# Optimization experiments

Hardware: AMD Instinct MI355X
Metric: run time of the kernel (lower is better)

## Reference

```python
import jax, jax.numpy as jnp
import numpy as np

NUM_BLKS = 6
H = 4
D = 64

def _ln(x, g, b, eps=1e-6):
    m = jnp.mean(x, -1, keepdims=True)
    v = jnp.mean((x - m) ** 2, -1, keepdims=True)
    return (x - m) * jax.lax.rsqrt(v + eps) * g + b

def _mlp3(x, W1, b1, W2, b2, W3, b3):
    h = jax.nn.gelu(x @ W1 + b1)
    h = jax.nn.gelu(h @ W2 + b2)
    return h @ W3 + b3

def _attn(q, kv, bias, kmask, Wq, Wk, Wv, Wo):
    B, Nq, Dm = q.shape
    Dh = Dm // H
    Q = (q @ Wq).reshape(B, Nq, H, Dh)
    K = (kv @ Wk).reshape(B, -1, H, Dh)
    V = (kv @ Wv).reshape(B, -1, H, Dh)
    logits = jnp.einsum('bqhd,bkhd->bhqk', Q, K) / jnp.sqrt(jnp.float32(Dh))
    logits = logits + bias[:, None]  # additive similarity-kernel bias
    logits = jnp.where(kmask[:, None, None, :], logits, -1e9)
    a = jax.nn.softmax(logits, -1)
    o = jnp.einsum('bhqk,bkhd->bqhd', a, V).reshape(B, Nq, Dm)
    return o @ Wo

def _bias(sim, p):
    # learned RBF-style bias; non-finite similarities masked to 0 (mirrors isfinite mask)
    return jnp.where(jnp.isfinite(sim), p[0] * jnp.exp(-sim * jax.nn.softplus(p[1])), 0.0)

def _forward(s_ctx, t_ctx, f_ctx, s_test, t_test, emb_obs, ea_W1, ea_b1, ea_W2, ea_b2, ea_W3, ea_b3, norm_g, norm_b, blk_Wq, blk_Wk, blk_Wv, blk_Wo, blk_ln1_g, blk_ln1_b, blk_ff_W1, blk_ff_b1, blk_ff_W2, blk_ff_b2, blk_ln2_g, blk_ln2_b, sbias_p, tbias_p, fnorm_g, fnorm_b, head_W1, head_b1, head_W2, head_b2, head_W3, head_b3, mask_ctx):
    B, NC, _ = f_ctx.shape
    NT = s_test.shape[1]
    obs_e = jnp.broadcast_to(emb_obs[1], (B, NC, emb_obs.shape[-1]))    # obs=1 embedding
    unobs_e = jnp.broadcast_to(emb_obs[0], (B, NT, emb_obs.shape[-1]))  # unobs=0 embedding
    f_test = jnp.zeros((B, NT, f_ctx.shape[-1]), f_ctx.dtype)
    ctx = jnp.concatenate([obs_e, s_ctx, t_ctx, f_ctx], -1)    # [B,NC,8]
    test = jnp.concatenate([unobs_e, s_test, t_test, f_test], -1)  # [B,NT,8]
    kvs = _ln(_mlp3(ctx, ea_W1, ea_b1, ea_W2, ea_b2, ea_W3, ea_b3), norm_g, norm_b)
    qvs = _ln(_mlp3(test, ea_W1, ea_b1, ea_W2, ea_b2, ea_W3, ea_b3), norm_g, norm_b)
    # pairwise similarity kernels (vmap over batch expressed via broadcasting)
    s_qk = jnp.sum((s_test[:, :, None] - s_ctx[:, None]) ** 2, -1)  # [B,NT,NC]
    s_kk = jnp.sum((s_ctx[:, :, None] - s_ctx[:, None]) ** 2, -1)   # [B,NC,NC]
    t_qk = jnp.abs(t_test[..., 0][:, :, None] - t_ctx[..., 0][:, None, :])
    t_kk = jnp.abs(t_ctx[..., 0][:, :, None] - t_ctx[..., 0][:, None, :])

    def _block(x, kv, bias, i):
        a = _attn(x, kv, bias, mask_ctx, blk_Wq[i], blk_Wk[i], blk_Wv[i], blk_Wo[i])
        x = _ln(x + a, blk_ln1_g[i], blk_ln1_b[i])
        h = jax.nn.gelu(x @ blk_ff_W1[i] + blk_ff_b1[i]) @ blk_ff_W2[i] + blk_ff_b2[i]
        return _ln(x + h, blk_ln2_g[i], blk_ln2_b[i])

    for i in range(NUM_BLKS):
        qk_b = _bias(s_qk, sbias_p[i]) + _bias(t_qk, tbias_p[i])
        kk_b = _bias(s_kk, sbias_p[i]) + _bias(t_kk, tbias_p[i])
        kvs = _block(kvs, kvs, kk_b, i)   # context self-attention
        qvs = _block(qvs, kvs, qk_b, i)   # test -> context cross-attention
    qvs = _ln(qvs, fnorm_g, fnorm_b)
    out = _mlp3(qvs, head_W1, head_b1, head_W2, head_b2, head_W3, head_b3)  # [B,NT,2]
    mean = out[..., :1]
    std = jax.nn.softplus(out[..., 1:]) + 1e-3  # DiagonalMVN params
    return jnp.concatenate([mean, std], -1)

def setup_inputs() -> dict:
    key = jax.random.key(0)
    ks = iter(jax.random.split(key, 48))
    rn = lambda *s: jax.random.normal(next(ks), s, jnp.float32)
    B, NC, NT = 8, 1024, 1024
    return dict(
        s_ctx=rn(B, NC, 2), t_ctx=rn(B, NC, 1), f_ctx=rn(B, NC, 1),
        mask_ctx=jnp.ones((B, NC), bool),
        s_test=rn(B, NT, 2), t_test=rn(B, NT, 1),
        emb_obs=rn(2, 4) * 0.02,
        ea_W1=rn(8, 256) * 0.05, ea_b1=jnp.zeros(256),
        ea_W2=rn(256, 128) * 0.05, ea_b2=jnp.zeros(128),
        ea_W3=rn(128, 64) * 0.05, ea_b3=jnp.zeros(64),
        norm_g=jnp.ones(64), norm_b=jnp.zeros(64),
        blk_Wq=rn(NUM_BLKS, D, D) * 0.05, blk_Wk=rn(NUM_BLKS, D, D) * 0.05,
        blk_Wv=rn(NUM_BLKS, D, D) * 0.05, blk_Wo=rn(NUM_BLKS, D, D) * 0.05,
        blk_ln1_g=jnp.ones((NUM_BLKS, D)), blk_ln1_b=jnp.zeros((NUM_BLKS, D)),
        blk_ff_W1=rn(NUM_BLKS, D, 4 * D) * 0.05, blk_ff_b1=jnp.zeros((NUM_BLKS, 4 * D)),
        blk_ff_W2=rn(NUM_BLKS, 4 * D, D) * 0.05, blk_ff_b2=jnp.zeros((NUM_BLKS, D)),
        blk_ln2_g=jnp.ones((NUM_BLKS, D)), blk_ln2_b=jnp.zeros((NUM_BLKS, D)),
        sbias_p=rn(NUM_BLKS, 2) * 0.5, tbias_p=rn(NUM_BLKS, 2) * 0.5,
        fnorm_g=jnp.ones(64), fnorm_b=jnp.zeros(64),
        head_W1=rn(64, 256) * 0.05, head_b1=jnp.zeros(256),
        head_W2=rn(256, 64) * 0.05, head_b2=jnp.zeros(64),
        head_W3=rn(64, 2) * 0.05, head_b3=jnp.zeros(2),
    )

def reference(s_ctx, t_ctx, f_ctx, mask_ctx, s_test, t_test, emb_obs, ea_W1, ea_b1, ea_W2, ea_b2, ea_W3, ea_b3, norm_g, norm_b, blk_Wq, blk_Wk, blk_Wv, blk_Wo, blk_ln1_g, blk_ln1_b, blk_ff_W1, blk_ff_b1, blk_ff_W2, blk_ff_b2, blk_ln2_g, blk_ln2_b, sbias_p, tbias_p, fnorm_g, fnorm_b, head_W1, head_b1, head_W2, head_b2, head_W3, head_b3):
    return _forward(s_ctx, t_ctx, f_ctx, s_test, t_test, emb_obs, ea_W1, ea_b1, ea_W2, ea_b2, ea_W3, ea_b3, norm_g, norm_b, blk_Wq, blk_Wk, blk_Wv, blk_Wo, blk_ln1_g, blk_ln1_b, blk_ff_W1, blk_ff_b1, blk_ff_W2, blk_ff_b2, blk_ln2_g, blk_ln2_b, sbias_p, tbias_p, fnorm_g, fnorm_b, head_W1, head_b1, head_W2, head_b2, head_W3, head_b3, mask_ctx)
```

## Files before the change

### kernel.cpp

```cpp
#include <hip/hip_runtime.h>
#include <hip/hip_bf16.h>

typedef __hip_bfloat16 bf16;

#define BB 8
#define NN 1024
#define HH 4

typedef __attribute__((ext_vector_type(4))) short s4v;
typedef __attribute__((ext_vector_type(4))) float f4v;
typedef __attribute__((ext_vector_type(8))) unsigned short us8v;

__device__ inline float b2f(bf16 x){ return __bfloat162float(x); }
__device__ inline float us2f(unsigned short u){
  union { unsigned int i; float f; } c; c.i = ((unsigned int)u) << 16; return c.f;
}
__device__ inline unsigned short f2us(float x){
  __hip_bfloat16 h = __float2bfloat16(x);
  union { __hip_bfloat16 h; unsigned short u; } c; c.h = h; return c.u;
}
__device__ inline float wsum(float v){
#pragma unroll
  for(int m=32;m>0;m>>=1) v += __shfl_xor(v,m,64);
  return v;
}
__device__ inline float tanh_f(float u){
  float e = __expf(-2.f*fabsf(u));
  float r = (1.f-e)/(1.f+e);
  return u < 0.f ? -r : r;
}
__device__ inline float gelu_f(float x){
  float u = 0.7978845608028654f*(x + 0.044715f*x*x*x);
  return 0.5f*x*(1.f+tanh_f(u));
}
__device__ inline float softplus_f(float x){
  return fmaxf(x,0.f) + log1pf(__expf(-fabsf(x)));
}

__global__ __launch_bounds__(256) void k_detect(const unsigned short* __restrict__ w,
                                                int n, int* __restrict__ flag){
  __shared__ int s;
  if(threadIdx.x==0) s=0;
  __syncthreads();
  int bad=0;
  for(int i=threadIdx.x;i<n;i+=256){
    float x = us2f(w[i]);
    if(!(fabsf(x) < 1000.f)) bad=1;
  }
  if(bad) atomicOr(&s,1);
  __syncthreads();
  if(threadIdx.x==0) *flag = s;
}

#define NSEG 36
struct ConvArgs {
  const void* src[NSEG];
  int dstoff[NSEG];
  int cum[NSEG+1];
};

__global__ __launch_bounds__(256) void k_convert(ConvArgs a, const int* __restrict__ flag,
                                                 unsigned short* __restrict__ dst){
  int f = *flag;
  int T = a.cum[NSEG];
  for(int i = blockIdx.x*256 + threadIdx.x; i < T; i += gridDim.x*256){
    int lo=0, hi=NSEG-1;
    while(lo<hi){ int mid=(lo+hi)>>1; if(i >= a.cum[mid+1]) lo=mid+1; else hi=mid; }
    int j = i - a.cum[lo];
    unsigned short v;
    if(f) v = f2us(((const float*)a.src[lo])[j]);
    else  v = ((const unsigned short*)a.src[lo])[j];
    dst[a.dstoff[lo] + j] = v;
  }
}

__global__ __launch_bounds__(256) void k_embed3(
    const bf16* __restrict__ s_ctx, const bf16* __restrict__ t_ctx, const bf16* __restrict__ f_ctx,
    const bf16* __restrict__ s_test, const bf16* __restrict__ t_test, const bf16* __restrict__ emb,
    const bf16* __restrict__ W1, const bf16* __restrict__ b1,
    const bf16* __restrict__ W2, const bf16* __restrict__ b2,
    const bf16* __restrict__ W3, const bf16* __restrict__ b3,
    const bf16* __restrict__ g, const bf16* __restrict__ bb,
    float* __restrict__ kvs, float* __restrict__ qvs)
{
  __shared__ float xs[32*8];
  __shared__ unsigned short h1b[32*264];
  __shared__ unsigned short h2b[32*136];
  __shared__ unsigned short wch[64*132];
  __shared__ unsigned short w3s[128*68];
  int tid=threadIdx.x, wv=tid>>6, lane=tid&63;
  int c=lane&15, quad=lane>>4;
  int tok0 = blockIdx.x*32;
  const f4v z4 = {0.f,0.f,0.f,0.f};

  {
    int t=tid>>3, i=tid&7;
    int tok=tok0+t;
    bool cx = tok < BB*NN; int n = cx? tok : tok-BB*NN;
    float v;
    if(i<4) v = b2f(emb[(cx?4:0)+i]);
    else if(i==4) v = b2f(cx? s_ctx[n*2] : s_test[n*2]);
    else if(i==5) v = b2f(cx? s_ctx[n*2+1] : s_test[n*2+1]);
    else if(i==6) v = b2f(cx? t_ctx[n] : t_test[n]);
    else v = cx? b2f(f_ctx[n]) : 0.f;
    xs[t*8+i]=v;
  }
  {
    const unsigned short* w3u=(const unsigned short*)W3;
    for(int v=tid; v<2048; v+=256){
      int k=v>>4, n4=(v&15)*4;
      ushort4 w = *(const ushort4*)&w3u[k*64+n4];
      *(ushort4*)&w3s[k*68+n4] = w;
    }
  }
  __syncthreads();

  {
    float w1r[8][4], b1r[4];
#pragma unroll
    for(int j=0;j<4;j++) b1r[j]=b2f(b1[lane+64*j]);
#pragma unroll
    for(int i=0;i<8;i++)
#pragma unroll
      for(int j=0;j<4;j++) w1r[i][j]=b2f(W1[i*256+lane+64*j]);
    for(int t=0;t<8;t++){
// ... 88 lines not shown
      float d=y-m;
      float vv=wsum(d*d)*(1.f/64.f);
      float o=d*rsqrtf(vv+1e-6f)*gg+b0;
      bool cx = tok<BB*NN; int bn = cx? tok : tok-BB*NN;
      (cx?kvs:qvs)[bn*64+lane]=o;
    }
  }
}

__global__ __launch_bounds__(256) void k_proj4(
  const float* __restrict__ x, const float* __restrict__ q2,
  const bf16* __restrict__ Wq, const bf16* __restrict__ Wk, const bf16* __restrict__ Wv,
  unsigned short* __restrict__ qA, unsigned short* __restrict__ kA,
  unsigned short* __restrict__ vA, unsigned short* __restrict__ qB)
{
  __shared__ float wq[4096], wk[4096], wv[4096];
  __shared__ float xs[1024], qs[1024];
  int tid = threadIdx.x;
  for(int v=tid; v<1536; v+=256){
    int m = v>>9;
    int idx = (v & 511) * 8;
    const unsigned short* src = (m==0)?(const unsigned short*)Wq
                              :((m==1)?(const unsigned short*)Wk:(const unsigned short*)Wv);
    us8v w = *(const us8v*)&src[idx];
    float* dst = (m==0)?wq:((m==1)?wk:wv);
#pragma unroll
    for(int e=0;e<8;e++) dst[idx+e] = us2f((unsigned short)w[e]);
  }
  int base = blockIdx.x*16;
  ((float4*)xs)[tid] = ((const float4*)(x  + (size_t)base*64))[tid];
  ((float4*)qs)[tid] = ((const float4*)(q2 + (size_t)base*64))[tid];
  __syncthreads();
  int wave=tid>>6, lane=tid&63;
  int h=lane>>4, dh=lane&15;
#pragma unroll
  for(int t=0;t<4;t++){
    int tl = wave*4+t;
    int tok = base+tl;
    int b = tok>>10, n = tok&1023;
    float aq=0.f, ak=0.f, av=0.f, aq2=0.f;
    for(int k=0;k<64;k++){
      float xv = xs[tl*64+k], qv = qs[tl*64+k];
      float wqv = wq[k*64+lane];
      aq += xv*wqv;
      ak += xv*wk[k*64+lane];
      av += xv*wv[k*64+lane];
      aq2 += qv*wqv;
    }
    int o = ((b*HH + h)*NN + n)*16 + dh;
    qA[o]=f2us(aq); kA[o]=f2us(ak); vA[o]=f2us(av); qB[o]=f2us(aq2);
  }
}

#define TSP 72
#define HSP 264
__global__ __launch_bounds__(256) void k_layer(
  const float* __restrict__ x,
  const unsigned short* __restrict__ qbh, const unsigned short* __restrict__ kbh,
  const unsigned short* __restrict__ vbh,
  const bf16* __restrict__ sq, const bf16* __restrict__ tq,
  const bf16* __restrict__ sk, const bf16* __restrict__ tk,
  const bf16* __restrict__ sp, const bf16* __restrict__ tp,
  const bf16* __restrict__ Wo, const bf16* __restrict__ g1, const bf16* __restrict__ b1,
  const bf16* __restrict__ W1, const bf16* __restrict__ fb1,
  const bf16* __restrict__ W2, const bf16* __restrict__ fb2,
  const bf16* __restrict__ g2, const bf16* __restrict__ b2g,
  float* __restrict__ xout, int mode,
  const bf16* __restrict__ Wm0, const bf16* __restrict__ Wm1,
  const bf16* __restrict__ Wm2, const bf16* __restrict__ Wm3,
  const bf16* __restrict__ Wm4,
  unsigned short* __restrict__ O0, unsigned short* __restrict__ O1,
  unsigned short* __restrict__ O2, unsigned short* __restrict__ O3,
  unsigned short* __restrict__ O4)
{
  __shared__ f4v arena4[3072];
  __shared__ unsigned short wos[4096];
  __shared__ float un[1024];
  __shared__ float ts[1024];
  __shared__ unsigned short tsb[16*TSP];
  __shared__ unsigned short hsb[16*HSP];
  __shared__ float ls[64];
  __shared__ float lmrg[4][16][4];
  unsigned short* arena_us = (unsigned short*)arena4;
  float* omrg = (float*)arena4;
  unsigned short* wbuf = arena_us + 8192;
  unsigned short* skbx = arena_us + 20480;
  unsigned short* skby = skbx + 1024;
  unsigned short* skbt = skby + 1024;

  int tid=threadIdx.x, wave=tid>>6, lane=tid&63;
  int c=lane&15, quad=lane>>4;
  int base = blockIdx.x*16;
  int b = base>>10, n0 = base&1023;
  const f4v z4 = {0.f,0.f,0.f,0.f};

  {
    const unsigned short* wou=(const unsigned short*)Wo;
    ((us8v*)wos)[tid] = ((const us8v*)wou)[tid];
    ((us8v*)wos)[tid+256] = ((const us8v*)wou)[tid+256];
    const unsigned short* usk=(const unsigned short*)sk;
    const unsigned short* utk=(const unsigned short*)tk;
    for(int i2=tid;i2<1024;i2+=256){
      int kg = b*NN + i2;
      skbx[i2]=usk[kg*2]; skby[i2]=usk[kg*2+1]; skbt[i2]=utk[kg];
    }
  }

  int qi = b*NN + n0 + c;
  float p0s=b2f(sp[0]), p1s=softplus_f(b2f(sp[1]));
  float p0t=b2f(tp[0]), p1t=softplus_f(b2f(tp[1]));
  float sq0=b2f(sq[qi*2]), sq1=b2f(sq[qi*2+1]), tq0=b2f(tq[qi]);
  s4v qf[4];
#pragma unroll
  for(int h=0;h<4;h++)
    qf[h] = *(const s4v*)(qbh + (size_t)((b*HH+h)*NN + n0 + c)*16 + quad*4);

  unsigned short* kstW = arena_us + wave*5120;
  unsigned short* vstW = kstW + 2560;

  f4v oacc[4]={z4,z4,z4,z4};
  float lacc[4]={0.f,0.f,0.f,0.f};

  ushort4 krg[2][4], vrg[2][4];
#pragma unroll
  for(int j=0;j<2;j++){
    int idx=lane+64*j; int h=idx>>5, key=idx&31;
    size_t src = ((size_t)(b*HH+h)*NN + wave*256 + key)*16;
    const ushort4* kp=(const ushort4*)(kbh+src);
    const ushort4* vp=(const ushort4*)(vbh+src);
#pragma unroll
    for(int e=0;e<4;e++){ krg[j][e]=kp[e]; vrg[j][e]=vp[e]; }
  }
  __syncthreads();

  for(int st=0; st<8; ++st){
    asm volatile("s_waitcnt lgkmcnt(0)" ::: "memory");
#pragma unroll
    for(int j=0;j<2;j++){
      int idx=lane+64*j; int h=idx>>5, key=idx&31;
      ushort4* kd = (ushort4*)&kstW[h*640 + key*20];
      kd[0]=krg[j][0]; kd[1]=krg[j][1]; kd[2]=krg[j][2]; kd[3]=krg[j][3];
      unsigned short* vd = &vstW[h*640 + key];
      vd[ 0*40]=vrg[j][0].x; vd[ 1*40]=vrg[j][0].y; vd[ 2*40]=vrg[j][0].z; vd[ 3*40]=vrg[j][0].w;
      vd[ 4*40]=vrg[j][1].x; vd[ 5*40]=vrg[j][1].y; vd[ 6*40]=vrg[j][1].z; vd[ 7*40]=vrg[j][1].w;
      vd[ 8*40]=vrg[j][2].x; vd[ 9*40]=vrg[j][2].y; vd[10*40]=vrg[j][2].z; vd[11*40]=vrg[j][2].w;
      vd[12*40]=vrg[j][3].x; vd[13*40]=vrg[j][3].y; vd[14*40]=vrg[j][3].z; vd[15*40]=vrg[j][3].w;
    }
    if(st<7){
#pragma unroll
      for(int j=0;j<2;j++){
        int idx=lane+64*j; int h=idx>>5, key=idx&31;
        size_t src = ((size_t)(b*HH+h)*NN + wave*256 + (st+1)*32 + key)*16;
        const ushort4* kp=(const ushort4*)(kbh+src);
        const ushort4* vp=(const ushort4*)(vbh+src);
#pragma unroll
        for(int e=0;e<4;e++){ krg[j][e]=kp[e]; vrg[j][e]=vp[e]; }
      }
    }
    asm volatile("s_waitcnt lgkmcnt(0)" ::: "memory");
    __builtin_amdgcn_sched_barrier(0);
#pragma unroll
    for(int t2=0;t2<2;t2++){
      int kk = st*32 + t2*16;
      float bias[4];
#pragma unroll
      for(int r=0;r<4;r++){
        int kix = wave*256 + kk + quad*4 + r;
        float d0 = sq0-us2f(skbx[kix]), d1 = sq1-us2f(skby[kix]);
        float dt = fabsf(tq0-us2f(skbt[kix]));
        bias[r] = p0s*__expf(-(d0*d0+d1*d1)*p1s) + p0t*__expf(-dt*p1t);
      }
#pragma unroll
      for(int h=0;h<4;h++){
        s4v kf = *(const s4v*)&kstW[h*640 + (t2*16+c)*20 + quad*4];
        f4v s = __builtin_amdgcn_mfma_f32_16x16x16bf16_1k(kf, qf[h], z4, 0,0,0);
        float p0 = __expf(fminf(s[0]*0.25f + bias[0], 60.f));
        float p1 = __expf(fminf(s[1]*0.25f + bias[1], 60.f));
        float p2 = __expf(fminf(s[2]*0.25f + bias[2], 60.f));
        float p3 = __expf(fminf(s[3]*0.25f + bias[3], 60.f));
        lacc[h] += (p0+p1)+(p2+p3);
        s4v pf;
        pf.x=(short)f2us(p0); pf.y=(short)f2us(p1);
        pf.z=(short)f2us(p2); pf.w=(short)f2us(p3);
        s4v vf = *(const s4v*)&vstW[h*640 + c*40 + t2*16 + quad*4];
        oacc[h] = __builtin_amdgcn_mfma_f32_16x16x16bf16_1k(vf, pf, oacc[h], 0,0,0);
      }
    }
  }

  __syncthreads();
#pragma unroll
  for(int h=0;h<4;h++){
    lacc[h] += __shfl_xor(lacc[h],16,64);
    lacc[h] += __shfl_xor(lacc[h],32,64);
  }
#pragma unroll
  for(int h=0;h<4;h++)
    *(f4v*)&omrg[(wave*16+c)*64 + h*16 + quad*4] = oacc[h];
  if(quad==0){
#pragma unroll
    for(int h=0;h<4;h++) lmrg[wave][c][h]=lacc[h];
  }
  {
    const unsigned short* w1u=(const unsigned short*)W1;
#pragma unroll
    for(int j=0;j<8;j++)
      ((us8v*)wbuf)[tid + j*256] = ((const us8v*)w1u)[tid + j*256];
  }
  __syncthreads();
  if(tid<64){
    int tl=tid>>2, h=tid&3;
    ls[tid] = lmrg[0][tl][h]+lmrg[1][tl][h]+lmrg[2][tl][h]+lmrg[3][tl][h];
  }
  __syncthreads();
#pragma unroll
  for(int j=0;j<4;j++){
    int i = j*256+tid;
    int tl=i>>6, hd=i&63;
    float o = omrg[tl*64+hd] + omrg[(16+tl)*64+hd]
            + omrg[(32+tl)*64+hd] + omrg[(48+tl)*64+hd];
    un[i] = o / ls[(tl<<2)|(hd>>4)];
  }
  __syncthreads();

  {
    float xr[4];
#pragma unroll
    for(int t=0;t<4;t++) xr[t] = x[(size_t)(base+wave*4+t)*64 + lane];
    float acc[4]={0.f,0.f,0.f,0.f};
    for(int k=0;k<64;k++){
      float w = us2f(wos[k*64+lane]);
      acc[0] += un[(wave*4+0)*64+k]*w;
      acc[1] += un[(wave*4+1)*64+k]*w;
      acc[2] += un[(wave*4+2)*64+k]*w;
      acc[3] += un[(wave*4+3)*64+k]*w;
    }
    float gg=b2f(g1[lane]), bbv=b2f(b1[lane]);
#pragma unroll
    for(int t=0;t<4;t++){
      float y = xr[t] + acc[t];
      float mm = wsum(y)*(1.f/64.f);
      float d = y-mm;
      float v = wsum(d*d)*(1.f/64.f);
      float tt = d*rsqrtf(v+1e-6f)*gg + bbv;
      ts[(wave*4+t)*64+lane] = tt;
      tsb[(wave*4+t)*TSP+lane] = f2us(tt);
    }
  }
  __syncthreads();

  {
    s4v af[4];
#pragma unroll
    for(int ks=0;ks<4;ks++)
      af[ks] = *(const s4v*)&tsb[c*TSP + ks*16 + quad*4];
#pragma unroll
    for(int tile=0;tile<4;tile++){
      int n0t = wave*64 + tile*16;
      f4v acc = z4;
#pragma unroll
      for(int ks=0;ks<4;ks++){
        int kb = ks*16 + quad*4;
        s4v bfv;
        bfv.x = (short)wbuf[(kb+0)*256 + n0t + c];
        bfv.y = (short)wbuf[(kb+1)*256 + n0t + c];
        bfv.z = (short)wbuf[(kb+2)*256 + n0t + c];
        bfv.w = (short)wbuf[(kb+3)*256 + n0t + c];
        acc = __builtin_amdgcn_mfma_f32_16x16x16bf16_1k(af[ks], bfv, acc, 0,0,0);
      }
      float bias = b2f(fb1[n0t + c]);
#pragma unroll
      for(int r=0;r<4;r++){
        int tok = quad*4 + r;
        hsb[tok*HSP + n0t + c] = f2us(gelu_f(acc[r] + bias));
      }
    }
  }
  __syncthreads();
  {
    const unsigned short* w2u=(const unsigned short*)W2;
#pragma unroll
    for(int j=0;j<8;j++)
      ((us8v*)wbuf)[tid + j*256] = ((const us8v*)w2u)[tid + j*256];
  }
  __syncthreads();

  {
    int n0t = wave*16;
    f4v acc = z4;
#pragma unroll
    for(int ks=0;ks<16;ks++){
      s4v af = *(const s4v*)&hsb[c*HSP + ks*16 + quad*4];
      int kb = ks*16 + quad*4;
      s4v bfv;
      bfv.x = (short)wbuf[(kb+0)*64 + n0t + c];
      bfv.y = (short)wbuf[(kb+1)*64 + n0t + c];
      bfv.z = (short)wbuf[(kb+2)*64 + n0t + c];
      bfv.w = (short)wbuf[(kb+3)*64 + n0t + c];
      acc = __builtin_amdgcn_mfma_f32_16x16x16bf16_1k(af, bfv, acc, 0,0,0);
    }
    float bias = b2f(fb2[n0t + c]);
#pragma unroll
    for(int r=0;r<4;r++)
      un[(quad*4+r)*64 + n0t + c] = acc[r] + bias;
  }
  __syncthreads();

  {
    float gg=b2f(g2[lane]), b0=b2f(b2g[lane]);
#pragma unroll
    for(int t=0;t<4;t++){
      float y = ts[(wave*4+t)*64+lane] + un[(wave*4+t)*64+lane];
      float mm = wsum(y)*(1.f/64.f);
      float d = y-mm;
      float v = wsum(d*d)*(1.f/64.f);
      float yo = d*rsqrtf(v+1e-6f)*gg + b0;
      xout[(size_t)(base+wave*4+t)*64+lane] = yo;
      ts[(wave*4+t)*64+lane] = yo;
    }
  }
  __syncthreads();

  if(mode==0){
#pragma unroll
    for(int j=0;j<2;j++){
      ((us8v*)wbuf)[tid + j*256       ] = ((const us8v*)(const unsigned short*)Wm0)[tid + j*256];
      ((us8v*)wbuf)[tid + j*256 +  512] = ((const us8v*)(const unsigned short*)Wm1)[tid + j*256];
      ((us8v*)wbuf)[tid + j*256 + 1024] = ((const us8v*)(const unsigned short*)Wm2)[tid + j*256];
      ((us8v*)wbuf)[tid + j*256 + 1536] = ((const us8v*)(const unsigned short*)Wm3)[tid + j*256];
      ((us8v*)wos )[tid + j*256       ] = ((const us8v*)(const unsigned short*)Wm4)[tid + j*256];
    }
  } else {
#pragma unroll
    for(int j=0;j<2;j++)
      ((us8v*)wos)[tid + j*256] = ((const us8v*)(const unsigned short*)Wm0)[tid + j*256];
  }
  __syncthreads();

  {
    int h=lane>>4, dh=lane&15;
    if(mode==0){
      float a0[4],a1[4],a2[4],a3[4],a4[4];
#pragma unroll
      for(int t=0;t<4;t++){ a0[t]=0.f;a1[t]=0.f;a2[t]=0.f;a3[t]=0.f;a4[t]=0.f; }
      for(int k=0;k<64;k++){
        float w0=us2f(wbuf[k*64+lane]);
        float w1=us2f(wbuf[4096+k*64+lane]);
        float w2=us2f(wbuf[8192+k*64+lane]);
        float w3=us2f(wbuf[12288+k*64+lane]);
        float w4=us2f(wos[k*64+lane]);
#pragma unroll
        for(int t=0;t<4;t++){
          float tv = ts[(wave*4+t)*64+k];
          a0[t]+=tv*w0; a1[t]+=tv*w1; a2[t]+=tv*w2; a3[t]+=tv*w3; a4[t]+=tv*w4;
        }
      }
#pragma unroll
      for(int t=0;t<4;t++){
        int tok = base+wave*4+t;
        int bq=tok>>10, n=tok&1023;
        int o = ((bq*HH+h)*NN+n)*16+dh;
        O0[o]=f2us(a0[t]); O1[o]=f2us(a1[t]); O2[o]=f2us(a2[t]);
        O3[o]=f2us(a3[t]); O4[o]=f2us(a4[t]);
      }
    } else {
      float a0[4]={0.f,0.f,0.f,0.f};
      for(int k=0;k<64;k++){
        float w0=us2f(wos[k*64+lane]);
#pragma unroll
        for(int t=0;t<4;t++) a0[t] += ts[(wave*4+t)*64+k]*w0;
      }
#pragma unroll
      for(int t=0;t<4;t++){
        int tok = base+wave*4+t;
        int bq=tok>>10, n=tok&1023;
        int o = ((bq*HH+h)*NN+n)*16+dh;
        O0[o]=f2us(a0[t]);
      }
    }
  }
}

__global__ __launch_bounds__(256) void k_head2(
  const float* __restrict__ qvs,
  const bf16* __restrict__ fng, const bf16* __restrict__ fnb,
  const bf16* __restrict__ W1, const bf16* __restrict__ b1,
  const bf16* __restrict__ W2, const bf16* __restrict__ b2,
  const bf16* __restrict__ W3, const bf16* __restrict__ b3,
  void* __restrict__ out, const int* __restrict__ flag)
{
  __shared__ unsigned short wbuf[16384];
  __shared__ float xls[1024];
  __shared__ float hh1[4096];
  int tid=threadIdx.x, wave=tid>>6, lane=tid&63;
  int base = blockIdx.x*16;
  {
    const unsigned short* w1u=(const unsigned short*)W1;
#pragma unroll
    for(int j=0;j<8;j++)
      ((us8v*)wbuf)[tid + j*256] = ((const us8v*)w1u)[tid + j*256];
  }
  {
    float gg=b2f(fng[lane]), bb=b2f(fnb[lane]);
#pragma unroll
    for(int t=0;t<4;t++){
      int tl=wave*4+t;
      float xv = qvs[(size_t)(base+tl)*64+lane];
      float m = wsum(xv)*(1.f/64.f);
      float d = xv-m;
      float v = wsum(d*d)*(1.f/64.f);
      xls[tl*64+lane] = d*rsqrtf(v+1e-6f)*gg + bb;
    }
  }
  __syncthreads();
  {
    float a0[4],a1[4],a2[4],a3[4];
    float bb0=b2f(b1[lane*4+0]), bb1v=b2f(b1[lane*4+1]),
          bb2v=b2f(b1[lane*4+2]), bb3=b2f(b1[lane*4+3]);
#pragma unroll
    for(int t=0;t<4;t++){ a0[t]=bb0; a1[t]=bb1v; a2[t]=bb2v; a3[t]=bb3; }
    for(int k=0;k<64;k++){
      ushort4 w = *(const ushort4*)&wbuf[k*256+lane*4];
      float w0=us2f(w.x), w1=us2f(w.y), w2=us2f(w.z), w3=us2f(w.w);
#pragma unroll
      for(int t=0;t<4;t++){
        float tv = xls[(wave*4+t)*64+k];
        a0[t]+=tv*w0; a1[t]+=tv*w1; a2[t]+=tv*w2; a3[t]+=tv*w3;
      }
    }
#pragma unroll
// ... 51 lines not shown

  ConvArgs ca;
  int cur = 0;
  int off[NSEG];
  {
    int cum = 0;
    for(int k=0;k<NSEG;k++){
      int n = in_sizes[idxs[k]];
      ca.src[k] = d_in[idxs[k]];
      ca.dstoff[k] = cur;
      ca.cum[k] = cum;
      off[k] = cur;
      cur += (n + 15) & ~15;
      cum += n;
    }
    ca.cum[NSEG] = cum;
  }
  size_t convEnd = 64 + (size_t)cur*2;
  size_t fbaseOff = (convEnd + 255) & ~255ULL;
  float* fbase = (float*)((char*)d_ws + fbaseOff);

  const bf16* P[NSEG];
  for(int k=0;k<NSEG;k++) P[k] = (const bf16*)(conv + off[k]);
  const bf16* s_ctx =P[0];  const bf16* t_ctx =P[1];  const bf16* f_ctx =P[2];
  const bf16* s_test=P[3];  const bf16* t_test=P[4];  const bf16* emb   =P[5];
  const bf16* eaW1=P[6];   const bf16* eab1=P[7];
  const bf16* eaW2=P[8];   const bf16* eab2=P[9];
  const bf16* eaW3=P[10];  const bf16* eab3=P[11];
  const bf16* ng=P[12];    const bf16* nb=P[13];
  const bf16* bWq=P[14];   const bf16* bWk=P[15];
  const bf16* bWv=P[16];   const bf16* bWo=P[17];
  const bf16* l1g=P[18];   const bf16* l1b=P[19];
  const bf16* fW1=P[20];   const bf16* fb1=P[21];
  const bf16* fW2=P[22];   const bf16* fb2=P[23];
  const bf16* l2g=P[24];   const bf16* l2b=P[25];
  const bf16* sbp=P[26];   const bf16* tbp=P[27];
  const bf16* fng=P[28];   const bf16* fnb=P[29];
  const bf16* hW1=P[30];   const bf16* hb1=P[31];
  const bf16* hW2=P[32];   const bf16* hb2=P[33];
  const bf16* hW3=P[34];   const bf16* hb3=P[35];

  float* kvs = fbase;
  float* qvs = fbase + 524288;
  unsigned short* qA0 = (unsigned short*)(fbase + 1048576);
  unsigned short* kA0 = (unsigned short*)(fbase + 1310720);
  unsigned short* vA0 = (unsigned short*)(fbase + 1572864);
  unsigned short* qB0 = (unsigned short*)(fbase + 1835008);
  unsigned short* kB  = (unsigned short*)(fbase + 2097152);
  unsigned short* vB  = (unsigned short*)(fbase + 2359296);
  unsigned short* qA1 = (unsigned short*)(fbase + 2621440);
  unsigned short* kA1 = (unsigned short*)(fbase + 2883584);
  unsigned short* vA1 = (unsigned short*)(fbase + 3145728);
  unsigned short* qB1 = (unsigned short*)(fbase + 3407872);

  k_detect<<<1,256,0,stream>>>((const unsigned short*)d_in[7], in_sizes[7], flagp);
  k_convert<<<512,256,0,stream>>>(ca, flagp, conv);
  k_embed3<<<512,256,0,stream>>>(s_ctx,t_ctx,f_ctx,s_test,t_test,emb,
                                 eaW1,eab1,eaW2,eab2,eaW3,eab3,ng,nb,kvs,qvs);
  k_proj4<<<512,256,0,stream>>>(kvs,qvs,bWq,bWk,bWv,qA0,kA0,vA0,qB0);

  unsigned short *qAc=qA0,*kAc=kA0,*vAc=vA0,*qBc=qB0;
  unsigned short *qAn=qA1,*kAn=kA1,*vAn=vA1,*qBn=qB1;

  for(int i=0;i<6;i++){
    int nx = (i<5)? i+1 : 5;
    const bf16* Wo=bWo+i*4096;
    const bf16* g1=l1g+i*64;   const bf16* b1=l1b+i*64;
    const bf16* W1=fW1+i*16384; const bf16* bb1=fb1+i*256;
    const bf16* W2=fW2+i*16384; const bf16* bb2=fb2+i*64;
    const bf16* g2=l2g+i*64;   const bf16* b2=l2b+i*64;
    const bf16* spi=sbp+i*2;   const bf16* tpi=tbp+i*2;
    const bf16* Wk_i=bWk+i*4096; const bf16* Wv_i=bWv+i*4096;
    const bf16* Wq_n=bWq+nx*4096; const bf16* Wk_n=bWk+nx*4096; const bf16* Wv_n=bWv+nx*4096;

    k_layer<<<512,256,0,stream>>>(kvs, qAc,kAc,vAc,
                                  s_ctx,t_ctx,s_ctx,t_ctx,spi,tpi,
                                  Wo,g1,b1,W1,bb1,W2,bb2,g2,b2, kvs, 0,
                                  Wk_i,Wv_i,Wq_n,Wk_n,Wv_n,
                                  kB,vB,qAn,kAn,vAn);
    k_layer<<<512,256,0,stream>>>(qvs, qBc,kB,vB,
                                  s_test,t_test,s_ctx,t_ctx,spi,tpi,
                                  Wo,g1,b1,W1,bb1,W2,bb2,g2,b2, qvs, 1,
                                  Wq_n,Wq_n,Wq_n,Wq_n,Wq_n,
                                  qBn,qBn,qBn,qBn,qBn);
    unsigned short* t;
    t=qAc; qAc=qAn; qAn=t;
    t=kAc; kAc=kAn; kAn=t;
    t=vAc; vAc=vAn; vAn=t;
    t=qBc; qBc=qBn; qBn=t;
  }
  k_head2<<<512,256,0,stream>>>(qvs,fng,fnb,hW1,hb1,hW2,hb2,hW3,hb3,d_out,flagp);
}
```

Measured before the change: 603.5 us.

## Pre-transpose swizzled layer weights, use MFMA for projections, and double block size to 512

```diff
diff --git a/kernel.cpp b/kernel.cpp
--- a/kernel.cpp
+++ b/kernel.cpp
@@ -71,6 +71,40 @@
     if(f) v = f2us(((const float*)a.src[lo])[j]);
     else  v = ((const unsigned short*)a.src[lo])[j];
     dst[a.dstoff[lo] + j] = v;
+  }
+}
+
+__global__ __launch_bounds__(256) void k_prep(
+  const bf16* __restrict__ Wo6, const bf16* __restrict__ Wq6,
+  const bf16* __restrict__ Wk6, const bf16* __restrict__ Wv6,
+  const bf16* __restrict__ W16, const bf16* __restrict__ W26,
+  unsigned short* __restrict__ out)
+{
+  int l = blockIdx.x / 6, m = blockIdx.x % 6;
+  int tid = threadIdx.x;
+  unsigned short* dst = out + l*49152;
+  if(m < 4){
+    const unsigned short* src = (const unsigned short*)
+      (m==0? Wo6 + l*4096 : m==1? Wq6 + l*4096 : m==2? Wk6 + l*4096 : Wv6 + l*4096);
+    unsigned short* d = dst + m*4096;
+    for(int e=tid; e<4096; e+=256){
+      int n = e>>6, k = e&63;
+      d[n*64 + (k ^ ((n&15)<<2))] = src[k*64 + n];
+    }
+  } else if(m==4){
+    const unsigned short* src = (const unsigned short*)(W16 + l*16384);
+    unsigned short* d = dst + 16384;
+    for(int e=tid; e<16384; e+=256){
+      int n = e>>6, k = e&63;
+      d[n*64 + (k ^ ((n&15)<<2))] = src[k*256 + n];
+    }
+  } else {
+    const unsigned short* src = (const unsigned short*)(W26 + l*16384);
+    unsigned short* d = dst + 32768;
+    for(int e=tid; e<16384; e+=256){
+      int n = e>>8, k = e&255;
+      d[n*256 + (k ^ ((n&15)<<2))] = src[k*64 + n];
+    }
   }
 }
 
@@ -265,37 +299,39 @@
   }
 }
 
-#define TSP 72
-#define HSP 264
-__global__ __launch_bounds__(256) void k_layer(
+#define HSP 260
+__global__ __launch_bounds__(512, 4) void k_layer(
   const float* __restrict__ x,
   const unsigned short* __restrict__ qbh, const unsigned short* __restrict__ kbh,
   const unsigned short* __restrict__ vbh,
   const bf16* __restrict__ sq, const bf16* __restrict__ tq,
   const bf16* __restrict__ sk, const bf16* __restrict__ tk,
   const bf16* __restrict__ sp, const bf16* __restrict__ tp,
-  const bf16* __restrict__ Wo, const bf16* __restrict__ g1, const bf16* __restrict__ b1,
-  const bf16* __restrict__ W1, const bf16* __restrict__ fb1,
-  const bf16* __restrict__ W2, const bf16* __restrict__ fb2,
+  const unsigned short* __restrict__ WoT,
+  const bf16* __restrict__ g1, const bf16* __restrict__ b1,
+  const unsigned short* __restrict__ W1T, const bf16* __restrict__ fb1,
+  const unsigned short* __restrict__ W2T, const bf16* __restrict__ fb2,
   const bf16* __restrict__ g2, const bf16* __restrict__ b2g,
   float* __restrict__ xout, int mode,
-  const bf16* __restrict__ Wm0, const bf16* __restrict__ Wm1,
-  const bf16* __restrict__ Wm2, const bf16* __restrict__ Wm3,
-  const bf16* __restrict__ Wm4,
+  const unsigned short* __restrict__ Wm0, const unsigned short* __restrict__ Wm1,
+  const unsigned short* __restrict__ Wm2, const unsigned short* __restrict__ Wm3,
+  const unsigned short* __restrict__ Wm4,
   unsigned short* __restrict__ O0, unsigned short* __restrict__ O1,
   unsigned short* __restrict__ O2, unsigned short* __restrict__ O3,
   unsigned short* __restrict__ O4)
 {
   __shared__ f4v arena4[3072];
   __shared__ unsigned short wos[4096];
-  __shared__ float un[1024];
   __shared__ float ts[1024];
-  __shared__ unsigned short tsb[16*TSP];
-  __shared__ unsigned short hsb[16*HSP];
+  __shared__ float lmrg[8][16][4];
   __shared__ float ls[64];
-  __shared__ float lmrg[4][16][4];
   unsigned short* arena_us = (unsigned short*)arena4;
   float* omrg = (float*)arena4;
+  unsigned short* unb = (unsigned short*)ts;
+  float* unWf = (float*)(arena_us + 3136);
+  unsigned short* hsb = arena_us;
+  float* unFf = (float*)(arena_us + 4160);
+  unsigned short* tsb = arena_us + 6240;
   unsigned short* wbuf = arena_us + 8192;
   unsigned short* skbx = arena_us + 20480;
   unsigned short* skby = skbx + 1024;
@@ -303,89 +339,77 @@
 
   int tid=threadIdx.x, wave=tid>>6, lane=tid&63;
   int c=lane&15, quad=lane>>4;
-  int base = blockIdx.x*16;
-  int b = base>>10, n0 = base&1023;
+  int base=blockIdx.x*16, bq=base>>10, ntok=base&1023;
   const f4v z4 = {0.f,0.f,0.f,0.f};
 
   {
-    const unsigned short* wou=(const unsigned short*)Wo;
-    ((us8v*)wos)[tid] = ((const us8v*)wou)[tid];
-    ((us8v*)wos)[tid+256] = ((const us8v*)wou)[tid+256];
+    ((us8v*)wos)[tid] = ((const us8v*)WoT)[tid];
     const unsigned short* usk=(const unsigned short*)sk;
     const unsigned short* utk=(const unsigned short*)tk;
-    for(int i2=tid;i2<1024;i2+=256){
-      int kg = b*NN + i2;
+    for(int i2=tid;i2<1024;i2+=512){
+      int kg = bq*NN + i2;
       skbx[i2]=usk[kg*2]; skby[i2]=usk[kg*2+1]; skbt[i2]=utk[kg];
     }
   }
 
-  int qi = b*NN + n0 + c;
+  int qi = bq*NN + ntok + c;
   float p0s=b2f(sp[0]), p1s=softplus_f(b2f(sp[1]));
   float p0t=b2f(tp[0]), p1t=softplus_f(b2f(tp[1]));
   float sq0=b2f(sq[qi*2]), sq1=b2f(sq[qi*2+1]), tq0=b2f(tq[qi]);
   s4v qf[4];
 #pragma unroll
   for(int h=0;h<4;h++)
-    qf[h] = *(const s4v*)(qbh + (size_t)((b*HH+h)*NN + n0 + c)*16 + quad*4);
-
-  unsigned short* kstW = arena_us + wave*5120;
-  unsigned short* vstW = kstW + 2560;
+    qf[h] = *(const s4v*)(qbh + (size_t)((bq*HH+h)*NN + ntok + c)*16 + quad*4);
+
+  unsigned short* kstW = arena_us + wave*2560;
+  unsigned short* vstW = kstW + 1280;
 
   f4v oacc[4]={z4,z4,z4,z4};
   float lacc[4]={0.f,0.f,0.f,0.f};
 
-  ushort4 krg[2][4], vrg[2][4];
-#pragma unroll
-  for(int j=0;j<2;j++){
-    int idx=lane+64*j; int h=idx>>5, key=idx&31;
-    size_t src = ((size_t)(b*HH+h)*NN + wave*256 + key)*16;
+  int hs = lane>>4, ky = lane&15;
+  ushort4 krg[4], vrg[4];
+  {
+    size_t src = ((size_t)(bq*HH+hs)*NN + wave*128 + ky)*16;
     const ushort4* kp=(const ushort4*)(kbh+src);
     const ushort4* vp=(const ushort4*)(vbh+src);
 #pragma unroll
-    for(int e=0;e<4;e++){ krg[j][e]=kp[e]; vrg[j][e]=vp[e]; }
+    for(int e=0;e<4;e++){ krg[e]=kp[e]; vrg[e]=vp[e]; }
   }
   __syncthreads();
 
   for(int st=0; st<8; ++st){
     asm volatile("s_waitcnt lgkmcnt(0)" ::: "memory");
-#pragma unroll
-    for(int j=0;j<2;j++){
-      int idx=lane+64*j; int h=idx>>5, key=idx&31;
-      ushort4* kd = (ushort4*)&kstW[h*640 + key*20];
-      kd[0]=krg[j][0]; kd[1]=krg[j][1]; kd[2]=krg[j][2]; kd[3]=krg[j][3];
-      unsigned short* vd = &vstW[h*640 + key];
-      vd[ 0*40]=vrg[j][0].x; vd[ 1*40]=vrg[j][0].y; vd[ 2*40]=vrg[j][0].z; vd[ 3*40]=vrg[j][0].w;
-      vd[ 4*40]=vrg[j][1].x; vd[ 5*40]=vrg[j][1].y; vd[ 6*40]=vrg[j][1].z; vd[ 7*40]=vrg[j][1].w;
-      vd[ 8*40]=vrg[j][2].x; vd[ 9*40]=vrg[j][2].y; vd[10*40]=vrg[j][2].z; vd[11*40]=vrg[j][2].w;
-      vd[12*40]=vrg[j][3].x; vd[13*40]=vrg[j][3].y; vd[14*40]=vrg[j][3].z; vd[15*40]=vrg[j][3].w;
+    {
+      ushort4* kd = (ushort4*)&kstW[hs*320 + ky*20];
+      kd[0]=krg[0]; kd[1]=krg[1]; kd[2]=krg[2]; kd[3]=krg[3];
+      unsigned short* vd = &vstW[hs*320 + ky];
+      vd[ 0*20]=vrg[0].x; vd[ 1*20]=vrg[0].y; vd[ 2*20]=vrg[0].z; vd[ 3*20]=vrg[0].w;
+      vd[ 4*20]=vrg[1].x; vd[ 5*20]=vrg[1].y; vd[ 6*20]=vrg[1].z; vd[ 7*20]=vrg[1].w;
+      vd[ 8*20]=vrg[2].x; vd[ 9*20]=vrg[2].y; vd[10*20]=vrg[2].z; vd[11*20]=vrg[2].w;
+      vd[12*20]=vrg[3].x; vd[13*20]=vrg[3].y; vd[14*20]=vrg[3].z; vd[15*20]=vrg[3].w;
     }
     if(st<7){
-#pragma unroll
-      for(int j=0;j<2;j++){
-        int idx=lane+64*j; int h=idx>>5, key=idx&31;
-        size_t src = ((size_t)(b*HH+h)*NN + wave*256 + (st+1)*32 + key)*16;
-        const ushort4* kp=(const ushort4*)(kbh+src);
-        const ushort4* vp=(const ushort4*)(vbh+src);
-#pragma unroll
-        for(int e=0;e<4;e++){ krg[j][e]=kp[e]; vrg[j][e]=vp[e]; }
-      }
+      size_t src = ((size_t)(bq*HH+hs)*NN + wave*128 + (st+1)*16 + ky)*16;
+      const ushort4* kp=(const ushort4*)(kbh+src);
+      const ushort4* vp=(const ushort4*)(vbh+src);
+#pragma unroll
+      for(int e=0;e<4;e++){ krg[e]=kp[e]; vrg[e]=vp[e]; }
     }
     asm volatile("s_waitcnt lgkmcnt(0)" ::: "memory");
     __builtin_amdgcn_sched_barrier(0);
-#pragma unroll
-    for(int t2=0;t2<2;t2++){
-      int kk = st*32 + t2*16;
+    {
       float bias[4];
 #pragma unroll
       for(int r=0;r<4;r++){
-        int kix = wave*256 + kk + quad*4 + r;
+        int kix = wave*128 + st*16 + quad*4 + r;
         float d0 = sq0-us2f(skbx[kix]), d1 = sq1-us2f(skby[kix]);
         float dt = fabsf(tq0-us2f(skbt[kix]));
         bias[r] = p0s*__expf(-(d0*d0+d1*d1)*p1s) + p0t*__expf(-dt*p1t);
       }
 #pragma unroll
       for(int h=0;h<4;h++){
-        s4v kf = *(const s4v*)&kstW[h*640 + (t2*16+c)*20 + quad*4];
+        s4v kf = *(const s4v*)&kstW[h*320 + c*20 + quad*4];
         f4v s = __builtin_amdgcn_mfma_f32_16x16x16bf16_1k(kf, qf[h], z4, 0,0,0);
         float p0 = __expf(fminf(s[0]*0.25f + bias[0], 60.f));
         float p1 = __expf(fminf(s[1]*0.25f + bias[1], 60.f));
@@ -395,200 +419,210 @@
         s4v pf;
         pf.x=(short)f2us(p0); pf.y=(short)f2us(p1);
         pf.z=(short)f2us(p2); pf.w=(short)f2us(p3);
-        s4v vf = *(const s4v*)&vstW[h*640 + c*40 + t2*16 + quad*4];
+        s4v vf = *(const s4v*)&vstW[h*320 + c*20 + quad*4];
         oacc[h] = __builtin_amdgcn_mfma_f32_16x16x16bf16_1k(vf, pf, oacc[h], 0,0,0);
       }
     }
   }
 
-  __syncthreads();
 #pragma unroll
   for(int h=0;h<4;h++){
     lacc[h] += __shfl_xor(lacc[h],16,64);
     lacc[h] += __shfl_xor(lacc[h],32,64);
   }
-#pragma unroll
-  for(int h=0;h<4;h++)
-    *(f4v*)&omrg[(wave*16+c)*64 + h*16 + quad*4] = oacc[h];
+
+  __syncthreads();
+  if(wave < 4){
+#pragma unroll
+    for(int h=0;h<4;h++)
+      *(f4v*)&omrg[wave*1024 + c*64 + h*16 + quad*4] = oacc[h];
+  }
   if(quad==0){
 #pragma unroll
     for(int h=0;h<4;h++) lmrg[wave][c][h]=lacc[h];
   }
   {
-    const unsigned short* w1u=(const unsigned short*)W1;
-#pragma unroll
-    for(int j=0;j<8;j++)
-      ((us8v*)wbuf)[tid + j*256] = ((const us8v*)w1u)[tid + j*256];
+#pragma unroll
+    for(int j=0;j<4;j++)
+      ((us8v*)wbuf)[tid + j*512] = ((const us8v*)W1T)[tid + j*512];
+  }
+  __syncthreads();
+  if(wave >= 4){
+#pragma unroll
+    for(int h=0;h<4;h++){
+      f4v* p = (f4v*)&omrg[(wave-4)*1024 + c*64 + h*16 + quad*4];
+      f4v cur = *p;
+      cur += oacc[h];
+      *p = cur;
+    }
   }
   __syncthreads();
   if(tid<64){
     int tl=tid>>2, h=tid&3;
-    ls[tid] = lmrg[0][tl][h]+lmrg[1][tl][h]+lmrg[2][tl][h]+lmrg[3][tl][h];
-  }
-  __syncthreads();
-#pragma unroll
-  for(int j=0;j<4;j++){
-    int i = j*256+tid;
+    float s=0.f;
+#pragma unroll
+    for(int w=0;w<8;w++) s += lmrg[w][tl][h];
+    ls[tid]=s;
+  }
+  __syncthreads();
+  for(int i=tid;i<1024;i+=512){
     int tl=i>>6, hd=i&63;
-    float o = omrg[tl*64+hd] + omrg[(16+tl)*64+hd]
-            + omrg[(32+tl)*64+hd] + omrg[(48+tl)*64+hd];
-    un[i] = o / ls[(tl<<2)|(hd>>4)];
-  }
-  __syncthreads();
-
-  {
-    float xr[4];
-#pragma unroll
-    for(int t=0;t<4;t++) xr[t] = x[(size_t)(base+wave*4+t)*64 + lane];
-    float acc[4]={0.f,0.f,0.f,0.f};
-    for(int k=0;k<64;k++){
-      float w = us2f(wos[k*64+lane]);
-      acc[0] += un[(wave*4+0)*64+k]*w;
-      acc[1] += un[(wave*4+1)*64+k]*w;
-      acc[2] += un[(wave*4+2)*64+k]*w;
-      acc[3] += un[(wave*4+3)*64+k]*w;
-    }
+    float o = omrg[i] + omrg[1024+i] + omrg[2048+i] + omrg[3072+i];
+    float val = o / ls[(tl<<2)|(hd>>4)];
+    unb[tl*68+hd]=f2us(val);
+  }
+  __syncthreads();
+  {
+    int tile=wave&3, khalf=wave>>2;
+    f4v acc=z4;
+#pragma unroll
+    for(int s2=0;s2<2;s2++){
+      int ks=khalf*2+s2;
+      s4v af = *(const s4v*)&unb[c*68 + ks*16 + quad*4];
+      int kb = ks*16 + quad*4;
+      s4v bfv = *(const s4v*)&wos[(tile*16+c)*64 + (kb ^ ((c&15)<<2))];
+      acc = __builtin_amdgcn_mfma_f32_16x16x16bf16_1k(af,bfv,acc,0,0,0);
+    }
+    if(khalf==0){
+#pragma unroll
+      for(int r=0;r<4;r++) unWf[(quad*4+r)*65 + tile*16 + c] = acc[r];
+    }
+    __syncthreads();
+    if(khalf==1){
+#pragma unroll
+      for(int r=0;r<4;r++) unWf[(quad*4+r)*65 + tile*16 + c] += acc[r];
+    }
+  }
+  __syncthreads();
+  {
     float gg=b2f(g1[lane]), bbv=b2f(b1[lane]);
 #pragma unroll
-    for(int t=0;t<4;t++){
-      float y = xr[t] + acc[t];
+    for(int t=0;t<2;t++){
+      int token=wave*2+t;
+      float y = x[(size_t)(base+token)*64 + lane] + unWf[token*65 + lane];
       float mm = wsum(y)*(1.f/64.f);
       float d = y-mm;
       float v = wsum(d*d)*(1.f/64.f);
       float tt = d*rsqrtf(v+1e-6f)*gg + bbv;
-      ts[(wave*4+t)*64+lane] = tt;
-      tsb[(wave*4+t)*TSP+lane] = f2us(tt);
-    }
-  }
-  __syncthreads();
-
+      ts[token*64+lane] = tt;
+      tsb[token*68+lane] = f2us(tt);
+    }
+  }
+  __syncthreads();
   {
     s4v af[4];
 #pragma unroll
     for(int ks=0;ks<4;ks++)
-      af[ks] = *(const s4v*)&tsb[c*TSP + ks*16 + quad*4];
-#pragma unroll
-    for(int tile=0;tile<4;tile++){
-      int n0t = wave*64 + tile*16;
+      af[ks] = *(const s4v*)&tsb[c*68 + ks*16 + quad*4];
+#pragma unroll
+    for(int tile=0;tile<2;tile++){
+      int n0t = wave*32 + tile*16;
       f4v acc = z4;
 #pragma unroll
       for(int ks=0;ks<4;ks++){
         int kb = ks*16 + quad*4;
-        s4v bfv;
-        bfv.x = (short)wbuf[(kb+0)*256 + n0t + c];
-        bfv.y = (short)wbuf[(kb+1)*256 + n0t + c];
-        bfv.z = (short)wbuf[(kb+2)*256 + n0t + c];
-        bfv.w = (short)wbuf[(kb+3)*256 + n0t + c];
-        acc = __builtin_amdgcn_mfma_f32_16x16x16bf16_1k(af[ks], bfv, acc, 0,0,0);
+        s4v bfv = *(const s4v*)&wbuf[(n0t+c)*64 + (kb ^ ((c&15)<<2))];
+        acc = __builtin_amdgcn_mfma_f32_16x16x16bf16_1k(af[ks],bfv,acc,0,0,0);
       }
       float bias = b2f(fb1[n0t + c]);
 #pragma unroll
-      for(int r=0;r<4;r++){
-        int tok = quad*4 + r;
-        hsb[tok*HSP + n0t + c] = f2us(gelu_f(acc[r] + bias));
-      }
-    }
-  }
-  __syncthreads();
-  {
-    const unsigned short* w2u=(const unsigned short*)W2;
-#pragma unroll
-    for(int j=0;j<8;j++)
-      ((us8v*)wbuf)[tid + j*256] = ((const us8v*)w2u)[tid + j*256];
-  }
-  __syncthreads();
-
-  {
-    int n0t = wave*16;
+      for(int r=0;r<4;r++)
+        hsb[(quad*4+r)*HSP + n0t + c] = f2us(gelu_f(acc[r] + bias));
+    }
+  }
+  __syncthreads();
+  {
+#pragma unroll
+    for(int j=0;j<4;j++)
+      ((us8v*)wbuf)[tid + j*512] = ((const us8v*)W2T)[tid + j*512];
+  }
+  __syncthreads();
+  {
+    int tile=wave&3, khalf=wave>>2;
+    int nb = tile*16;
     f4v acc = z4;
 #pragma unroll
-    for(int ks=0;ks<16;ks++){
-      s4v af = *(const s4v*)&hsb[c*HSP + ks*16 + quad*4];
-      int kb = ks*16 + quad*4;
-      s4v bfv;
-      bfv.x = (short)wbuf[(kb+0)*64 + n0t + c];
-      bfv.y = (short)wbuf[(kb+1)*64 + n0t + c];
-      bfv.z = (short)wbuf[(kb+2)*64 + n0t + c];
-      bfv.w = (short)wbuf[(kb+3)*64 + n0t + c];
-      acc = __builtin_amdgcn_mfma_f32_16x16x16bf16_1k(af, bfv, acc, 0,0,0);
-    }
-    float bias = b2f(fb2[n0t + c]);
-#pragma unroll
-    for(int r=0;r<4;r++)
-      un[(quad*4+r)*64 + n0t + c] = acc[r] + bias;
-  }
-  __syncthreads();
-
+    for(int s2=0;s2<8;s2++){
+      int ksg = khalf*8 + s2;
+      s4v af = *(const s4v*)&hsb[c*HSP + ksg*16 + quad*4];
+      int kb = ksg*16 + quad*4;
+      s4v bfv = *(const s4v*)&wbuf[(nb+c)*256 + (kb ^ ((c&15)<<2))];
+      acc = __builtin_amdgcn_mfma_f32_16x16x16bf16_1k(af,bfv,acc,0,0,0);
+    }
+    if(khalf==0){
+      float bias = b2f(fb2[nb+c]);
+#pragma unroll
+      for(int r=0;r<4;r++) unFf[(quad*4+r)*65 + nb + c] = acc[r] + bias;
+    }
+    __syncthreads();
+    if(khalf==1){
+#pragma unroll
+      for(int r=0;r<4;r++) unFf[(quad*4+r)*65 + nb + c] += acc[r];
+    }
+  }
+  __syncthreads();
   {
     float gg=b2f(g2[lane]), b0=b2f(b2g[lane]);
 #pragma unroll
-    for(int t=0;t<4;t++){
-      float y = ts[(wave*4+t)*64+lane] + un[(wave*4+t)*64+lane];
+    for(int t=0;t<2;t++){
+      int token=wave*2+t;
+      float y = ts[token*64+lane] + unFf[token*65+lane];
       float mm = wsum(y)*(1.f/64.f);
       float d = y-mm;
       float v = wsum(d*d)*(1.f/64.f);
       float yo = d*rsqrtf(v+1e-6f)*gg + b0;
-      xout[(size_t)(base+wave*4+t)*64+lane] = yo;
-      ts[(wave*4+t)*64+lane] = yo;
-    }
-  }
-  __syncthreads();
-
-  if(mode==0){
-#pragma unroll
-    for(int j=0;j<2;j++){
-      ((us8v*)wbuf)[tid + j*256       ] = ((const us8v*)(const unsigned short*)Wm0)[tid + j*256];
-      ((us8v*)wbuf)[tid + j*256 +  512] = ((const us8v*)(const unsigned short*)Wm1)[tid + j*256];
-      ((us8v*)wbuf)[tid + j*256 + 1024] = ((const us8v*)(const unsigned short*)Wm2)[tid + j*256];
-      ((us8v*)wbuf)[tid + j*256 + 1536] = ((const us8v*)(const unsigned short*)Wm3)[tid + j*256];
-      ((us8v*)wos )[tid + j*256       ] = ((const us8v*)(const unsigned short*)Wm4)[tid + j*256];
-    }
-  } else {
-#pragma unroll
-    for(int j=0;j<2;j++)
-      ((us8v*)wos)[tid + j*256] = ((const us8v*)(const unsigned short*)Wm0)[tid + j*256];
-  }
-  __syncthreads();
-
-  {
-    int h=lane>>4, dh=lane&15;
+      xout[(size_t)(base+token)*64+lane] = yo;
+      tsb[token*68+lane] = f2us(yo);
+    }
     if(mode==0){
-      float a0[4],a1[4],a2[4],a3[4],a4[4];
-#pragma unroll
-      for(int t=0;t<4;t++){ a0[t]=0.f;a1[t]=0.f;a2[t]=0.f;a3[t]=0.f;a4[t]=0.f; }
-      for(int k=0;k<64;k++){
-        float w0=us2f(wbuf[k*64+lane]);
-        float w1=us2f(wbuf[4096+k*64+lane]);
-        float w2=us2f(wbuf[8192+k*64+lane]);
-        float w3=us2f(wbuf[12288+k*64+lane]);
-        float w4=us2f(wos[k*64+lane]);
-#pragma unroll
-        for(int t=0;t<4;t++){
-          float tv = ts[(wave*4+t)*64+k];
-          a0[t]+=tv*w0; a1[t]+=tv*w1; a2[t]+=tv*w2; a3[t]+=tv*w3; a4[t]+=tv*w4;
+      ((us8v*)wbuf)[tid        ] = ((const us8v*)Wm0)[tid];
+      ((us8v*)wbuf)[tid +  512 ] = ((const us8v*)Wm1)[tid];
+      ((us8v*)wbuf)[tid + 1024 ] = ((const us8v*)Wm2)[tid];
+      ((us8v*)wbuf)[tid + 1536 ] = ((const us8v*)Wm3)[tid];
+      ((us8v*)wos )[tid        ] = ((const us8v*)Wm4)[tid];
+    } else {
+      ((us8v*)wos )[tid        ] = ((const us8v*)Wm0)[tid];
+    }
+  }
+  __syncthreads();
+  {
+    s4v af[4];
+#pragma unroll
+    for(int ks=0;ks<4;ks++)
+      af[ks] = *(const s4v*)&tsb[c*68 + ks*16 + quad*4];
+    if(mode==0){
+#pragma unroll
+      for(int j=0;j<3;j++){
+        int p = wave + 8*j;
+        if(p < 20){
+          int m = p>>2, tile = p&3;
+          const unsigned short* wsrc = (m<4)? (wbuf + m*4096) : wos;
+          unsigned short* Op = (m==0)?O0:((m==1)?O1:((m==2)?O2:((m==3)?O3:O4)));
+          f4v acc = z4;
+#pragma unroll
+          for(int ks=0;ks<4;ks++){
+            int kb = ks*16 + quad*4;
+            s4v bfv = *(const s4v*)&wsrc[(tile*16+c)*64 + (kb ^ ((c&15)<<2))];
+            acc = __builtin_amdgcn_mfma_f32_16x16x16bf16_1k(af[ks],bfv,acc,0,0,0);
+          }
+#pragma unroll
+          for(int r=0;r<4;r++)
+            Op[((size_t)(bq*HH + tile)*NN + ntok + quad*4 + r)*16 + c] = f2us(acc[r]);
         }
       }
-#pragma unroll
-      for(int t=0;t<4;t++){
-        int tok = base+wave*4+t;
-        int bq=tok>>10, n=tok&1023;
-        int o = ((bq*HH+h)*NN+n)*16+dh;
-        O0[o]=f2us(a0[t]); O1[o]=f2us(a1[t]); O2[o]=f2us(a2[t]);
-        O3[o]=f2us(a3[t]); O4[o]=f2us(a4[t]);
-      }
     } else {
-      float a0[4]={0.f,0.f,0.f,0.f};
-      for(int k=0;k<64;k++){
-        float w0=us2f(wos[k*64+lane]);
-#pragma unroll
-        for(int t=0;t<4;t++) a0[t] += ts[(wave*4+t)*64+k]*w0;
-      }
-#pragma unroll
-      for(int t=0;t<4;t++){
-        int tok = base+wave*4+t;
-        int bq=tok>>10, n=tok&1023;
-        int o = ((bq*HH+h)*NN+n)*16+dh;
-        O0[o]=f2us(a0[t]);
+      if(wave < 4){
+        int tile = wave;
+        f4v acc = z4;
+#pragma unroll
+        for(int ks=0;ks<4;ks++){
+          int kb = ks*16 + quad*4;
+          s4v bfv = *(const s4v*)&wos[(tile*16+c)*64 + (kb ^ ((c&15)<<2))];
+          acc = __builtin_amdgcn_mfma_f32_16x16x16bf16_1k(af[ks],bfv,acc,0,0,0);
+        }
+#pragma unroll
+        for(int r=0;r<4;r++)
+          O0[((size_t)(bq*HH + tile)*NN + ntok + quad*4 + r)*16 + c] = f2us(acc[r]);
       }
     }
   }
@@ -746,9 +780,11 @@
   unsigned short* kA1 = (unsigned short*)(fbase + 2883584);
   unsigned short* vA1 = (unsigned short*)(fbase + 3145728);
   unsigned short* qB1 = (unsigned short*)(fbase + 3407872);
+  unsigned short* prepT = (unsigned short*)(fbase + 3670016);
 
   k_detect<<<1,256,0,stream>>>((const unsigned short*)d_in[7], in_sizes[7], flagp);
   k_convert<<<512,256,0,stream>>>(ca, flagp, conv);
+  k_prep<<<36,256,0,stream>>>(bWo,bWq,bWk,bWv,fW1,fW2,prepT);
   k_embed3<<<512,256,0,stream>>>(s_ctx,t_ctx,f_ctx,s_test,t_test,emb,
                                  eaW1,eab1,eaW2,eab2,eaW3,eab3,ng,nb,kvs,qvs);
   k_proj4<<<512,256,0,stream>>>(kvs,qvs,bWq,bWk,bWv,qA0,kA0,vA0,qB0);
@@ -758,24 +794,30 @@
 
   for(int i=0;i<6;i++){
     int nx = (i<5)? i+1 : 5;
-    const bf16* Wo=bWo+i*4096;
+    const unsigned short* Lp = prepT + i*49152;
+    const unsigned short* Np = prepT + nx*49152;
+    const unsigned short* WoT = Lp;
+    const unsigned short* W1T = Lp + 16384;
+    const unsigned short* W2T = Lp + 32768;
+    const unsigned short* WqTn = Np + 4096;
+    const unsigned short* WkTi = Lp + 8192;
+    const unsigned short* WvTi = Lp + 12288;
+    const unsigned short* WkTn = Np + 8192;
+    const unsigned short* WvTn = Np + 12288;
     const bf16* g1=l1g+i*64;   const bf16* b1=l1b+i*64;
-    const bf16* W1=fW1+i*16384; const bf16* bb1=fb1+i*256;
-    const bf16* W2=fW2+i*16384; const bf16* bb2=fb2+i*64;
+    const bf16* bb1=fb1+i*256; const bf16* bb2=fb2+i*64;
     const bf16* g2=l2g+i*64;   const bf16* b2=l2b+i*64;
     const bf16* spi=sbp+i*2;   const bf16* tpi=tbp+i*2;
-    const bf16* Wk_i=bWk+i*4096; const bf16* Wv_i=bWv+i*4096;
-    const bf16* Wq_n=bWq+nx*4096; const bf16* Wk_n=bWk+nx*4096; const bf16* Wv_n=bWv+nx*4096;
-
-    k_layer<<<512,256,0,stream>>>(kvs, qAc,kAc,vAc,
+
+    k_layer<<<512,512,0,stream>>>(kvs, qAc,kAc,vAc,
                                   s_ctx,t_ctx,s_ctx,t_ctx,spi,tpi,
-                                  Wo,g1,b1,W1,bb1,W2,bb2,g2,b2, kvs, 0,
-                                  Wk_i,Wv_i,Wq_n,Wk_n,Wv_n,
+                                  WoT,g1,b1,W1T,bb1,W2T,bb2,g2,b2, kvs, 0,
+                                  WkTi,WvTi,WqTn,WkTn,WvTn,
                                   kB,vB,qAn,kAn,vAn);
-    k_layer<<<512,256,0,stream>>>(qvs, qBc,kB,vB,
+    k_layer<<<512,512,0,stream>>>(qvs, qBc,kB,vB,
                                   s_test,t_test,s_ctx,t_ctx,spi,tpi,
-                                  Wo,g1,b1,W1,bb1,W2,bb2,g2,b2, qvs, 1,
-                                  Wq_n,Wq_n,Wq_n,Wq_n,Wq_n,
+                                  WoT,g1,b1,W1T,bb1,W2T,bb2,g2,b2, qvs, 1,
+                                  WqTn,WqTn,WqTn,WqTn,WqTn,
                                   qBn,qBn,qBn,qBn,qBn);
     unsigned short* t;
     t=qAc; qAc=qAn; qAn=t;
```

Result: faster. 519.8 us (-13.9%).
